# Performance work log

Measured on AMD Instinct MI355X. Metric: run time of the kernel, lower is better.

Reference implementation:

```python
import jax, jax.numpy as jnp
import numpy as np


def trilinear_sample(x, pts):
    """F.grid_sample 3D, mode='bilinear' (trilinear), padding_mode='border', align_corners=True.
    x: [B,C,D,H,W]; pts: [B,P,3] normalized coords in (x,y,z)=(W,H,D) order. Returns [B,C,P]."""
    B, C, D, H, W = x.shape

    def unnorm(g, size):
        # align_corners=True mapping, border padding = clamp coordinate
        return jnp.clip((g + 1.0) * 0.5 * (size - 1), 0.0, size - 1.0)

    ix = unnorm(pts[..., 0], W)
    iy = unnorm(pts[..., 1], H)
    iz = unnorm(pts[..., 2], D)
    x0 = jnp.floor(ix); y0 = jnp.floor(iy); z0 = jnp.floor(iz)
    fx = (ix - x0)[:, None, :]; fy = (iy - y0)[:, None, :]; fz = (iz - z0)[:, None, :]
    x0i = x0.astype(jnp.int32); y0i = y0.astype(jnp.int32); z0i = z0.astype(jnp.int32)
    x1i = jnp.minimum(x0i + 1, W - 1)
    y1i = jnp.minimum(y0i + 1, H - 1)
    z1i = jnp.minimum(z0i + 1, D - 1)

    xf = x.reshape(B, C, D * H * W)

    def gather(zi, yi, xi):
        idx = (zi * H + yi) * W + xi  # [B,P]
        return jnp.take_along_axis(xf, idx[:, None, :], axis=2)  # [B,C,P]

    wx0 = 1.0 - fx; wx1 = fx
    wy0 = 1.0 - fy; wy1 = fy
    wz0 = 1.0 - fz; wz1 = fz
    out = (gather(z0i, y0i, x0i) * wz0 * wy0 * wx0
           + gather(z0i, y0i, x1i) * wz0 * wy0 * wx1
           + gather(z0i, y1i, x0i) * wz0 * wy1 * wx0
           + gather(z0i, y1i, x1i) * wz0 * wy1 * wx1
           + gather(z1i, y0i, x0i) * wz1 * wy0 * wx0
           + gather(z1i, y0i, x1i) * wz1 * wy0 * wx1
           + gather(z1i, y1i, x0i) * wz1 * wy1 * wx0
           + gather(z1i, y1i, x1i) * wz1 * wy1 * wx1)
    return out


def setup_inputs() -> dict:
    key = jax.random.key(0)
    ks = jax.random.split(key, 12)
    B, C, G, N, K = 2, 64, 64, 50000, 8
    Cin = C + 3          # point_head / neighbour_head input channels
    Cd = C + 3 + 4       # delta conv input channels (features + coords + shape)
    s = 0.05
    x = jax.random.normal(ks[0], (B, C, G, G, G), jnp.float32)
    vertices = jax.random.uniform(ks[1], (B, N, 3), jnp.float32, -1.0, 1.0)
    shape_w = jax.random.normal(ks[2], (4, 4), jnp.float32) * s
    shape_b = jax.random.normal(ks[3], (4,), jnp.float32) * s
    # original init fills delta weights with 0; use small random values for a non-degenerate test
    delta_w = jax.random.normal(ks[4], (K * 3, Cd), jnp.float32) * 0.01
    delta_b = jax.random.normal(ks[5], (K * 3,), jnp.float32) * 0.01
    ph_w = jax.random.normal(ks[6], (C, Cin), jnp.float32) * s
    ph_b = jax.random.normal(ks[7], (C,), jnp.float32) * s
    nh1_w = jax.random.normal(ks[8], (C, Cin), jnp.float32) * s
    nh1_b = jax.random.normal(ks[9], (C,), jnp.float32) * s
    nh2_w = jax.random.normal(ks[10], (C, C, K + 1), jnp.float32) * s  # Conv2d kernel (1, K+1), no bias
    return {"x": x, "vertices": vertices, "shape_w": shape_w, "shape_b": shape_b,
            "delta_w": delta_w, "delta_b": delta_b, "ph_w": ph_w, "ph_b": ph_b,
            "nh1_w": nh1_w, "nh1_b": nh1_b, "nh2_w": nh2_w}


def reference(x, vertices, shape_w, shape_b, delta_w, delta_b, ph_w, ph_b, nh1_w, nh1_b, nh2_w):
    B, C, D, H, W = x.shape
    N = vertices.shape[1]
    K = delta_w.shape[0] // 3

    # sample point features
    xp = trilinear_sample(x, vertices)                                   # [B,C,N]
    cpoints = jnp.concatenate([xp, vertices.transpose(0, 2, 1)], axis=1)  # [B,C+3,N]

    # point head: 1x1 conv == per-point linear
    pfeat = jnp.einsum('oc,bcn->bno', ph_w, cpoints) + ph_b               # [B,N,C]

    # shape conditioning
    shape_vec = jnp.array([C, D, H, W], jnp.float32) @ shape_w.T + shape_b  # [4]
    sfeat = jnp.broadcast_to(shape_vec[None, :, None], (B, 4, N))
    feats = jnp.concatenate([cpoints, sfeat], axis=1)                     # [B,C+7,N]

    # learned neighbour offsets
    delta = (jnp.einsum('oc,bcn->bno', delta_w, feats) + delta_b).reshape(B, N, K, 3)
    nbrs = vertices[:, :, None, :] + delta                                # [B,N,K,3]

    # sample neighbour features
    xn = trilinear_sample(x, nbrs.reshape(B, N * K, 3)).reshape(B, C, N, K)
    cnb = jnp.concatenate([xn, nbrs.transpose(0, 3, 1, 2)], axis=1)       # [B,C+3,N,K]
    nin = jnp.concatenate([cpoints[..., None], cnb], axis=-1)             # [B,C+3,N,K+1]

    # neighbour head: 1x1 conv -> GELU -> (1,K+1) conv (reduces the K+1 axis)
    h = jax.nn.gelu(jnp.einsum('oc,bcnk->bonk', nh1_w, nin)
                    + nh1_b[None, :, None, None], approximate=False)
    nfeat = jnp.einsum('ock,bcnk->bno', nh2_w, h)                         # [B,N,C]

    return pfeat + nfeat
```

## Files before the change

### kernel.cpp

```cpp
#include <hip/hip_runtime.h>
#include <math.h>

constexpr int Bc = 2, Cc = 64, Nc = 50000, Kc = 8;
constexpr int PT = 16;
constexpr int NBLK = (Bc * Nc) / PT;

constexpr int BIAS_PH = 16;
constexpr int BIAS_N1 = 272;
constexpr int BIAS_DL = 528;
constexpr int B_PH  = 1024;
constexpr int B_N1  = 13312;
constexpr int B_DH  = 25600;
constexpr int B_DLO = 31744;
constexpr int B_N2  = 37888;
constexpr size_t XT_BYTE = 262144;
constexpr size_t XT_USHORTS = (size_t)Bc * 64 * 64 * 64 * 64;

using bf16x8 = __attribute__((ext_vector_type(8))) short;
using f32x4  = __attribute__((ext_vector_type(4))) float;

__device__ __forceinline__ float gelu_exact(float v) {
    return 0.5f * v * (1.0f + erff(v * 0.70710678118654752f));
}
__device__ __forceinline__ float gelu_fast(float v) {
    float u = fmaf(0.044715f * v * v, v, v);
    float s = 1.0f / (1.0f + __expf(-1.5957691216057308f * u));
    return v * s;
}
__device__ __forceinline__ ushort f2bf(float f) {
    unsigned u = __float_as_uint(f);
    unsigned r = (u + 0x7FFFu + ((u >> 16) & 1u)) >> 16;
    return (ushort)r;
}
__device__ __forceinline__ float bf2f(ushort u) {
    return __uint_as_float(((unsigned)u) << 16);
}
__device__ __forceinline__ float tri8(float v000, float v001, float v010, float v011,
                                      float v100, float v101, float v110, float v111,
                                      float fx, float fy, float fz) {
    float c00 = fmaf(fx, v001 - v000, v000);
    float c01 = fmaf(fx, v011 - v010, v010);
    float c10 = fmaf(fx, v101 - v100, v100);
    float c11 = fmaf(fx, v101 - v100, v100);
    c11 = fmaf(fx, v111 - v110, v110);
    float c0  = fmaf(fy, c01 - c00, c00);
    float c1  = fmaf(fy, c11 - c10, c10);
    return fmaf(fz, c1 - c0, c0);
}

__device__ __forceinline__ void precompute_pt(int* __restrict__ smp, int p,
                                              float nx, float ny, float nz) {
    float ix = fminf(fmaxf((nx + 1.0f) * 31.5f, 0.0f), 63.0f);
    float iy = fminf(fmaxf((ny + 1.0f) * 31.5f, 0.0f), 63.0f);
    float iz = fminf(fmaxf((nz + 1.0f) * 31.5f, 0.0f), 63.0f);
    float fx0 = floorf(ix), fy0 = floorf(iy), fz0 = floorf(iz);
    int x0 = (int)fx0, y0 = (int)fy0, z0 = (int)fz0;
    smp[p*8+0] = ((z0 << 12) + (y0 << 6) + x0) << 5;
    smp[p*8+1] = (x0 < 63) ? 32 : 0;
    smp[p*8+2] = (y0 < 63) ? 2048 : 0;
    smp[p*8+3] = (z0 < 63) ? 131072 : 0;
    smp[p*8+4] = __float_as_int(ix - fx0);
    smp[p*8+5] = __float_as_int(iy - fy0);
    smp[p*8+6] = __float_as_int(iz - fz0);
}

__device__ __forceinline__ void sample_pair2(const unsigned* __restrict__ xtb32,
                                             ushort* __restrict__ stage,
                                             const int* __restrict__ smp,
                                             int cp, int p) {
    const int* s = smp + p * 8;
    int base = s[0], dx = s[1], dy = s[2], dz = s[3];
    float fx = __int_as_float(s[4]);
    float fy = __int_as_float(s[5]);
    float fz = __int_as_float(s[6]);
    const unsigned* r = xtb32 + base + cp;
    unsigned u000 = r[0],       u001 = r[dx];
    unsigned u010 = r[dy],      u011 = r[dy + dx];
    unsigned u100 = r[dz],      u101 = r[dz + dx];
    unsigned u110 = r[dz + dy], u111 = r[dz + dy + dx];
    float sa = tri8(bf2f((ushort)u000), bf2f((ushort)u001),
                    bf2f((ushort)u010), bf2f((ushort)u011),
                    bf2f((ushort)u100), bf2f((ushort)u101),
                    bf2f((ushort)u110), bf2f((ushort)u111), fx, fy, fz);
    float sb = tri8(bf2f((ushort)(u000 >> 16)), bf2f((ushort)(u001 >> 16)),
                    bf2f((ushort)(u010 >> 16)), bf2f((ushort)(u011 >> 16)),
                    bf2f((ushort)(u100 >> 16)), bf2f((ushort)(u101 >> 16)),
                    bf2f((ushort)(u110 >> 16)), bf2f((ushort)(u111 >> 16)), fx, fy, fz);
    *(unsigned*)(stage + p * 104 + 2 * cp) =
        (unsigned)f2bf(sa) | ((unsigned)f2bf(sb) << 16);
}

__device__ __forceinline__ float sample_cm(const float* __restrict__ xb,
                                           float gx, float gy, float gz) {
    float ix = fminf(fmaxf((gx + 1.0f) * 31.5f, 0.0f), 63.0f);
    float iy = fminf(fmaxf((gy + 1.0f) * 31.5f, 0.0f), 63.0f);
    float iz = fminf(fmaxf((gz + 1.0f) * 31.5f, 0.0f), 63.0f);
    float fx0 = floorf(ix), fy0 = floorf(iy), fz0 = floorf(iz);
    int x0 = (int)fx0, y0 = (int)fy0, z0 = (int)fz0;
    float fx = ix - fx0, fy = iy - fy0, fz = iz - fz0;
    int x1 = (x0 < 63) ? x0 + 1 : 63;
    int dy = (y0 < 63) ? 64 : 0;
    int dz = (z0 < 63) ? 4096 : 0;
    const float* r = xb + ((z0 << 12) + (y0 << 6));
    float v000 = r[x0],           v001 = r[x1];
    float v010 = r[x0 + dy],      v011 = r[x1 + dy];
    float v100 = r[x0 + dz],      v101 = r[x1 + dz];
    float v110 = r[x0 + dy + dz], v111 = r[x1 + dy + dz];
    float c00 = fmaf(fx, v001 - v000, v000);
    float c01 = fmaf(fx, v011 - v010, v010);
    float c10 = fmaf(fx, v101 - v100, v100);
    float c11 = fmaf(fx, v111 - v110, v110);
    float c0  = fmaf(fy, c01 - c00, c00);
    float c1  = fmaf(fy, c11 - c10, c10);
    return fmaf(fz, c1 - c0, c0);
}

__global__ void sb_pack(const float* __restrict__ shape_w, const float* __restrict__ shape_b,
                        const float* __restrict__ delta_w, const float* __restrict__ delta_b,
                        const float* __restrict__ ph_w, const float* __restrict__ ph_b,
                        const float* __restrict__ nh1_w, const float* __restrict__ nh1_b,
                        const float* __restrict__ nh2_w, char* __restrict__ wsb) {
    int tid = blockIdx.x * blockDim.x + threadIdx.x;
    int nt  = gridDim.x * blockDim.x;
    float*  bph = (float*)(wsb + BIAS_PH);
    float*  bn1 = (float*)(wsb + BIAS_N1);
    float*  bdl = (float*)(wsb + BIAS_DL);
    ushort* wph = (ushort*)(wsb + B_PH);
    ushort* wn1 = (ushort*)(wsb + B_N1);
    ushort* wdh = (ushort*)(wsb + B_DH);
    ushort* wdl = (ushort*)(wsb + B_DLO);
    ushort* wn2 = (ushort*)(wsb + B_N2);

    for (int e = tid; e < 64; e += nt) { bph[e] = ph_b[e]; bn1[e] = nh1_b[e]; }
    for (int e = tid; e < 32; e += nt) {
        float v = 0.0f;
        if (e < 24) {
            v = delta_b[e];
#pragma unroll
            for (int i = 0; i < 4; ++i) {
                float sv = 64.0f * (shape_w[i*4] + shape_w[i*4+1] + shape_w[i*4+2] + shape_w[i*4+3])
                         + shape_b[i];
                v += sv * delta_w[e * 71 + 67 + i];
            }
        }
        bdl[e] = v;
    }
    for (int e = tid; e < 6144; e += nt) {
        int frag = e >> 9, lane = (e >> 3) & 63, j = e & 7;
        int kt = frag >> 2, n = frag & 3;
        int k = kt * 32 + ((lane >> 4) << 3) + j;
        int col = n * 16 + (lane & 15);
        wph[e] = (k < 67) ? f2bf(ph_w[col * 67 + k])  : (ushort)0;
        wn1[e] = (k < 67) ? f2bf(nh1_w[col * 67 + k]) : (ushort)0;
    }
    for (int e = tid; e < 3072; e += nt) {
        int frag = e >> 9, lane = (e >> 3) & 63, j = e & 7;
        int kt = frag >> 1, n = frag & 1;
        int k = kt * 32 + ((lane >> 4) << 3) + j;
        int col = n * 16 + (lane & 15);
        float w = (col < 24 && k < 67) ? delta_w[col * 71 + k] : 0.0f;
        ushort hi = f2bf(w);
        wdh[e] = hi;
        wdl[e] = f2bf(w - bf2f(hi));
    }
    for (int e = tid; e < 36864; e += nt) {
        int frag = e >> 9, lane = (e >> 3) & 63, j = e & 7;
        int c9 = frag >> 3, kt = (frag >> 2) & 1, n = frag & 3;
        int k = kt * 32 + ((lane >> 4) << 3) + j;
        int c = n * 16 + (lane & 15);
        wn2[e] = f2bf(nh2_w[(c * 64 + k) * 9 + c9]);
    }
}

__global__ __launch_bounds__(256) void sb_transpose(const float* __restrict__ x,
                                                    ushort* __restrict__ xt) {
    __shared__ float tile[64][65];
    int blk = blockIdx.x;
    int b = blk >> 12, zy = blk & 4095;
    const float* __restrict__ src = x + ((size_t)b << 24) + zy * 64;
    unsigned* __restrict__ dst32 = (unsigned*)(xt + ((size_t)b << 24) + (size_t)zy * 4096);
    int t = threadIdx.x;
    int xx = t & 63, c0 = t >> 6;
#pragma unroll
    for (int i = 0; i < 16; ++i) {
        int c = i * 4 + c0;
        tile[c][xx] = src[((size_t)c << 18) + xx];
    }
    __syncthreads();
    int cp = t & 31, xs0 = t >> 5;
#pragma unroll
    for (int i = 0; i < 8; ++i) {
        int xs = i * 8 + xs0;
        unsigned lo = f2bf(tile[cp * 2][xs]);
        unsigned hi = f2bf(tile[cp * 2 + 1][xs]);
        dst32[xs * 32 + cp] = lo | (hi << 16);
    }
}

__global__ __launch_bounds__(64, 6) void sb_main_mfma(
        const ushort* __restrict__ xt, const float* __restrict__ verts,
        const char* __restrict__ wsb, float* __restrict__ out) {
    __shared__ __align__(16) ushort stage[PT * 104];
    __shared__ __align__(16) ushort hst[PT * 72];
    __shared__ float pfs[PT * 64];
    __shared__ float cst[PT * 4];
    __shared__ float dls[PT * 32];
    __shared__ __align__(16) int smp[PT * 8];

    const int lane = threadIdx.x;
    const int l15 = lane & 15, lg = lane >> 4;
    const int half8 = (lane >> 5) * 8;
    const int cp = lane & 31;
    const int g0 = blockIdx.x * PT;
    const int b  = g0 / Nc;
    const unsigned* __restrict__ xtb32 = (const unsigned*)(xt + ((size_t)b << 24));

    const float*  bph = (const float*)(wsb + BIAS_PH);
    const float*  bn1 = (const float*)(wsb + BIAS_N1);
    const float*  bdl = (const float*)(wsb + BIAS_DL);
    const ushort* Wph = (const ushort*)(wsb + B_PH);
    const ushort* Wn1 = (const ushort*)(wsb + B_N1);
    const ushort* Wdh = (const ushort*)(wsb + B_DH);
    const ushort* Wdl = (const ushort*)(wsb + B_DLO);
    const ushort* Wn2 = (const ushort*)(wsb + B_N2);

#pragma unroll
    for (int i = 0; i < (PT * 104) / 64; ++i) stage[i * 64 + lane] = 0;

    if (lane < PT) {
        const float* vp = verts + (size_t)(g0 + lane) * 3;
        float x = vp[0], y = vp[1], z = vp[2];
        cst[lane*4+0] = x; cst[lane*4+1] = y; cst[lane*4+2] = z;
        uint4 cw;
        cw.x = (unsigned)f2bf(x) | ((unsigned)f2bf(y) << 16);
        cw.y = (unsigned)f2bf(z);
        cw.z = 0u; cw.w = 0u;
        *(uint4*)(stage + lane * 104 + 64) = cw;
        precompute_pt(smp, lane, x, y, z);
    }
    __syncthreads();

#pragma unroll 4
    for (int pp = 0; pp < 8; ++pp)
        sample_pair2(xtb32, stage, smp, cp, half8 + pp);
    __syncthreads();

    {
        f32x4 pf[4], dd[2];
#pragma unroll
        for (int n = 0; n < 4; ++n) {
            float bp = bph[n*16 + l15];
            pf[n] = (f32x4){bp, bp, bp, bp};
        }
#pragma unroll
        for (int n = 0; n < 2; ++n) {
            float bd = bdl[n*16 + l15];
            dd[n] = (f32x4){bd, bd, bd, bd};
        }
        __builtin_amdgcn_s_setprio(1);
#pragma unroll
        for (int kt = 0; kt < 3; ++kt) {
            bf16x8 a = *(const bf16x8*)(stage + l15 * 104 + kt * 32 + lg * 8);
#pragma unroll
            for (int n = 0; n < 4; ++n) {
                bf16x8 bw = *(const bf16x8*)(Wph + ((kt*4 + n) << 9) + lane * 8);
                pf[n] = __builtin_amdgcn_mfma_f32_16x16x32_bf16(a, bw, pf[n], 0, 0, 0);
            }
#pragma unroll
            for (int n = 0; n < 2; ++n) {
                bf16x8 bh = *(const bf16x8*)(Wdh + ((kt*2 + n) << 9) + lane * 8);
                dd[n] = __builtin_amdgcn_mfma_f32_16x16x32_bf16(a, bh, dd[n], 0, 0, 0);
                bf16x8 bl = *(const bf16x8*)(Wdl + ((kt*2 + n) << 9) + lane * 8);
                dd[n] = __builtin_amdgcn_mfma_f32_16x16x32_bf16(a, bl, dd[n], 0, 0, 0);
            }
        }
        __builtin_amdgcn_s_setprio(0);
#pragma unroll
        for (int n = 0; n < 2; ++n)
#pragma unroll
            for (int r = 0; r < 4; ++r)
                dls[(lg*4 + r) * 32 + n*16 + l15] = dd[n][r];
#pragma unroll
        for (int n = 0; n < 4; ++n)
#pragma unroll
            for (int r = 0; r < 4; ++r)
                pfs[(lg*4 + r) * 64 + n*16 + l15] = pf[n][r];
    }

    {
        f32x4 hh[4];
#pragma unroll
        for (int n = 0; n < 4; ++n) {
            float bh = bn1[n*16 + l15];
            hh[n] = (f32x4){bh, bh, bh, bh};
        }
        __builtin_amdgcn_s_setprio(1);
#pragma unroll
        for (int kt = 0; kt < 3; ++kt) {
            bf16x8 a = *(const bf16x8*)(stage + l15 * 104 + kt * 32 + lg * 8);
#pragma unroll
            for (int n = 0; n < 4; ++n) {
                bf16x8 b1 = *(const bf16x8*)(Wn1 + ((kt*4 + n) << 9) + lane * 8);
                hh[n] = __builtin_amdgcn_mfma_f32_16x16x32_bf16(a, b1, hh[n], 0, 0, 0);
            }
        }
        __builtin_amdgcn_s_setprio(0);
#pragma unroll
        for (int n = 0; n < 4; ++n)
#pragma unroll
            for (int r = 0; r < 4; ++r)
                hst[(lg*4 + r) * 72 + n*16 + l15] = f2bf(gelu_fast(hh[n][r]));
    }
    __syncthreads();

    f32x4 nf[4];
#pragma unroll
    for (int n = 0; n < 4; ++n) nf[n] = (f32x4){0.f, 0.f, 0.f, 0.f};
    __builtin_amdgcn_s_setprio(1);
#pragma unroll
    for (int kt = 0; kt < 2; ++kt) {
        bf16x8 a = *(const bf16x8*)(hst + l15 * 72 + kt * 32 + lg * 8);
#pragma unroll
        for (int n = 0; n < 4; ++n) {
            bf16x8 bw = *(const bf16x8*)(Wn2 + ((kt*4 + n) << 9) + lane * 8);
            nf[n] = __builtin_amdgcn_mfma_f32_16x16x32_bf16(a, bw, nf[n], 0, 0, 0);
        }
    }
    __builtin_amdgcn_s_setprio(0);

    for (int k = 0; k < Kc; ++k) {
        if (lane < PT) {
            float x = cst[lane*4+0] + dls[lane*32 + 3*k + 0];
            float y = cst[lane*4+1] + dls[lane*32 + 3*k + 1];
            float z = cst[lane*4+2] + dls[lane*32 + 3*k + 2];
            uint4 cw;
            cw.x = (unsigned)f2bf(x) | ((unsigned)f2bf(y) << 16);
            cw.y = (unsigned)f2bf(z);
            cw.z = 0u; cw.w = 0u;
            *(uint4*)(stage + lane * 104 + 64) = cw;
            precompute_pt(smp, lane, x, y, z);
        }
#pragma unroll 4
        for (int pp = 0; pp < 8; ++pp)
            sample_pair2(xtb32, stage, smp, cp, half8 + pp);
        __syncthreads();

        f32x4 hk[4];
#pragma unroll
        for (int n = 0; n < 4; ++n) {
            float bh = bn1[n*16 + l15];
            hk[n] = (f32x4){bh, bh, bh, bh};
        }
        __builtin_amdgcn_s_setprio(1);
#pragma unroll
        for (int kt = 0; kt < 3; ++kt) {
            bf16x8 a = *(const bf16x8*)(stage + l15 * 104 + kt * 32 + lg * 8);
#pragma unroll
            for (int n = 0; n < 4; ++n) {
                bf16x8 b1 = *(const bf16x8*)(Wn1 + ((kt*4 + n) << 9) + lane * 8);
                hk[n] = __builtin_amdgcn_mfma_f32_16x16x32_bf16(a, b1, hk[n], 0, 0, 0);
            }
        }
        __builtin_amdgcn_s_setprio(0);
#pragma unroll
        for (int n = 0; n < 4; ++n)
#pragma unroll
            for (int r = 0; r < 4; ++r)
                hst[(lg*4 + r) * 72 + n*16 + l15] = f2bf(gelu_fast(hk[n][r]));
        __syncthreads();

        const ushort* Wk = Wn2 + ((size_t)(k + 1) << 12);
        __builtin_amdgcn_s_setprio(1);
#pragma unroll
        for (int kt = 0; kt < 2; ++kt) {
            bf16x8 a = *(const bf16x8*)(hst + l15 * 72 + kt * 32 + lg * 8);
#pragma unroll
            for (int n = 0; n < 4; ++n) {
                bf16x8 bw = *(const bf16x8*)(Wk + ((kt*4 + n) << 9) + lane * 8);
                nf[n] = __builtin_amdgcn_mfma_f32_16x16x32_bf16(a, bw, nf[n], 0, 0, 0);
            }
        }
        __builtin_amdgcn_s_setprio(0);
    }

#pragma unroll
    for (int n = 0; n < 4; ++n)
#pragma unroll
        for (int r = 0; r < 4; ++r)
            out[(size_t)(g0 + lg*4 + r) * 64 + n*16 + l15] =
                pfs[(lg*4 + r) * 64 + n*16 + l15] + nf[n][r];
}

__global__ __launch_bounds__(64) void sb_fallback(
        const float* __restrict__ x, const float* __restrict__ verts,
        const float* __restrict__ shape_w, const float* __restrict__ shape_b,
        const float* __restrict__ delta_w, const float* __restrict__ delta_b,
        const float* __restrict__ ph_w, const float* __restrict__ ph_b,
        const float* __restrict__ nh1_w, const float* __restrict__ nh1_b,
        const float* __restrict__ nh2_w, float* __restrict__ out) {
    __shared__ float cp[72];
    __shared__ float hcol[64];
    __shared__ float dl[24];
    int lane = threadIdx.x;
    int g = blockIdx.x;
    int b = g / Nc;
    const float* xb = x + ((size_t)(b * 64 + lane) << 18);
    float vx = verts[g*3], vy = verts[g*3+1], vz = verts[g*3+2];
    cp[lane] = sample_cm(xb, vx, vy, vz);
    if (lane < 8) {
        float v = 0.0f;
        if      (lane == 0) v = vx;
        else if (lane == 1) v = vy;
        else if (lane == 2) v = vz;
        else if (lane < 7) {
            int i = lane - 3;
            v = 64.0f*(shape_w[i*4]+shape_w[i*4+1]+shape_w[i*4+2]+shape_w[i*4+3]) + shape_b[i];
        }
        cp[64 + lane] = v;
    }
    __syncthreads();
    float pfv = ph_b[lane];
    for (int j = 0; j < 67; ++j) pfv += ph_w[lane*67 + j] * cp[j];
    if (lane < 24) {
        float s = delta_b[lane];
        for (int j = 0; j < 71; ++j) s += delta_w[lane*71 + j] * cp[j];
        dl[lane] = s;
    }
    float h = nh1_b[lane];
    for (int j = 0; j < 67; ++j) h += nh1_w[lane*67 + j] * cp[j];
    hcol[lane] = gelu_exact(h);
    __syncthreads();
    float nfv = 0.0f;
    for (int c2 = 0; c2 < 64; ++c2) nfv += nh2_w[(lane*64 + c2)*9] * hcol[c2];
    for (int k = 0; k < 8; ++k) {
        __syncthreads();
        float nx = vx + dl[3*k], ny = vy + dl[3*k+1], nz = vz + dl[3*k+2];
        cp[lane] = sample_cm(xb, nx, ny, nz);
        if (lane < 3) cp[64 + lane] = (lane == 0) ? nx : (lane == 1) ? ny : nz;
        __syncthreads();
        float hv = nh1_b[lane];
        for (int j = 0; j < 67; ++j) hv += nh1_w[lane*67 + j] * cp[j];
        hcol[lane] = gelu_exact(hv);
        __syncthreads();
        for (int c2 = 0; c2 < 64; ++c2) nfv += nh2_w[(lane*64 + c2)*9 + k + 1] * hcol[c2];
    }
    out[(size_t)g * 64 + lane] = pfv + nfv;
}

extern "C" void kernel_launch(void* const* d_in, const int* in_sizes, int n_in,
                              void* d_out, int out_size, void* d_ws, size_t ws_size,
                              hipStream_t stream) {
    const float* x       = (const float*)d_in[0];
    const float* verts   = (const float*)d_in[1];
    const float* shape_w = (const float*)d_in[2];
    const float* shape_b = (const float*)d_in[3];
    const float* delta_w = (const float*)d_in[4];
    const float* delta_b = (const float*)d_in[5];
    const float* ph_w    = (const float*)d_in[6];
    const float* ph_b    = (const float*)d_in[7];
    const float* nh1_w   = (const float*)d_in[8];
    const float* nh1_b   = (const float*)d_in[9];
    const float* nh2_w   = (const float*)d_in[10];
    float* out = (float*)d_out;
    char*  wsb = (char*)d_ws;

    const size_t need = XT_BYTE + XT_USHORTS * 2;
    if (ws_size >= need) {
        ushort* xt = (ushort*)(wsb + XT_BYTE);
        sb_pack<<<96, 256, 0, stream>>>(shape_w, shape_b, delta_w, delta_b,
                                        ph_w, ph_b, nh1_w, nh1_b, nh2_w, wsb);
        sb_transpose<<<Bc * 4096, 256, 0, stream>>>(x, xt);
        sb_main_mfma<<<NBLK, 64, 0, stream>>>(xt, verts, wsb, out);
    } else {
        sb_fallback<<<Bc * Nc, 64, 0, stream>>>(x, verts, shape_w, shape_b, delta_w, delta_b,
                                                ph_w, ph_b, nh1_w, nh1_b, nh2_w, out);
    }
}
```

Baseline: 215.9 us.

## Prefetch trilinear corner gathers into LDS asynchronously, overlapping with MFMA work

Replaces the per-neighbour synchronous gather-and-interpolate with global_load_lds async copies of the corner values into an LDS raw buffer. The next neighbour's gathers are issued before the current neighbour's MFMA layers run, and sampling metadata is double-buffered. The point-linear result now stays in registers instead of LDS. This adds an LDS buffer and more live registers, and the occupancy hint is lowered from 6 to 4 waves.

```diff
diff --git a/kernel.cpp b/kernel.cpp
--- a/kernel.cpp
+++ b/kernel.cpp
@@ -41,11 +41,16 @@
     float c00 = fmaf(fx, v001 - v000, v000);
     float c01 = fmaf(fx, v011 - v010, v010);
     float c10 = fmaf(fx, v101 - v100, v100);
-    float c11 = fmaf(fx, v101 - v100, v100);
-    c11 = fmaf(fx, v111 - v110, v110);
+    float c11 = fmaf(fx, v111 - v110, v110);
     float c0  = fmaf(fy, c01 - c00, c00);
     float c1  = fmaf(fy, c11 - c10, c10);
     return fmaf(fz, c1 - c0, c0);
+}
+
+__device__ __forceinline__ void gll_dword(const unsigned* g, ushort* l) {
+    __builtin_amdgcn_global_load_lds(
+        (const __attribute__((address_space(1))) unsigned*)(g),
+        (__attribute__((address_space(3))) unsigned*)(l), 4, 0, 0);
 }
 
 __device__ __forceinline__ void precompute_pt(int* __restrict__ smp, int p,
@@ -55,39 +60,73 @@
     float iz = fminf(fmaxf((nz + 1.0f) * 31.5f, 0.0f), 63.0f);
     float fx0 = floorf(ix), fy0 = floorf(iy), fz0 = floorf(iz);
     int x0 = (int)fx0, y0 = (int)fy0, z0 = (int)fz0;
-    smp[p*8+0] = ((z0 << 12) + (y0 << 6) + x0) << 5;
-    smp[p*8+1] = (x0 < 63) ? 32 : 0;
-    smp[p*8+2] = (y0 < 63) ? 2048 : 0;
-    smp[p*8+3] = (z0 < 63) ? 131072 : 0;
-    smp[p*8+4] = __float_as_int(ix - fx0);
-    smp[p*8+5] = __float_as_int(iy - fy0);
-    smp[p*8+6] = __float_as_int(iz - fz0);
-}
-
-__device__ __forceinline__ void sample_pair2(const unsigned* __restrict__ xtb32,
-                                             ushort* __restrict__ stage,
-                                             const int* __restrict__ smp,
-                                             int cp, int p) {
-    const int* s = smp + p * 8;
-    int base = s[0], dx = s[1], dy = s[2], dz = s[3];
-    float fx = __int_as_float(s[4]);
-    float fy = __int_as_float(s[5]);
-    float fz = __int_as_float(s[6]);
-    const unsigned* r = xtb32 + base + cp;
-    unsigned u000 = r[0],       u001 = r[dx];
-    unsigned u010 = r[dy],      u011 = r[dy + dx];
-    unsigned u100 = r[dz],      u101 = r[dz + dx];
-    unsigned u110 = r[dz + dy], u111 = r[dz + dy + dx];
-    float sa = tri8(bf2f((ushort)u000), bf2f((ushort)u001),
-                    bf2f((ushort)u010), bf2f((ushort)u011),
-                    bf2f((ushort)u100), bf2f((ushort)u101),
-                    bf2f((ushort)u110), bf2f((ushort)u111), fx, fy, fz);
-    float sb = tri8(bf2f((ushort)(u000 >> 16)), bf2f((ushort)(u001 >> 16)),
-                    bf2f((ushort)(u010 >> 16)), bf2f((ushort)(u011 >> 16)),
-                    bf2f((ushort)(u100 >> 16)), bf2f((ushort)(u101 >> 16)),
-                    bf2f((ushort)(u110 >> 16)), bf2f((ushort)(u111 >> 16)), fx, fy, fz);
-    *(unsigned*)(stage + p * 104 + 2 * cp) =
-        (unsigned)f2bf(sa) | ((unsigned)f2bf(sb) << 16);
+    int* s = smp + p * 12;
+    s[0] = ((z0 << 12) + (y0 << 6) + x0) << 5;
+    s[1] = (x0 < 63) ? 32 : 0;
+    s[2] = (y0 < 63) ? 2048 : 0;
+    s[3] = (z0 < 63) ? 131072 : 0;
+    s[4] = __float_as_int(ix - fx0);
+    s[5] = __float_as_int(iy - fy0);
+    s[6] = __float_as_int(iz - fz0);
+    s[7] = __float_as_int(nx);
+    s[8] = __float_as_int(ny);
+    s[9] = __float_as_int(nz);
+}
+
+__device__ __forceinline__ void issue_all(const unsigned* __restrict__ xtb32,
+                                          ushort* __restrict__ raw,
+                                          const int* __restrict__ smp, int lane) {
+    int xs = (lane >= 32);
+    int chp = lane & 31;
+#pragma unroll 4
+    for (int p = 0; p < PT; ++p) {
+        const int* s = smp + p * 12;
+        int base = s[0], dxo = s[1], dyo = s[2], dzo = s[3];
+        const unsigned* g = xtb32 + base + (xs ? dxo : 0) + chp;
+        ushort* rp = raw + p * 512;
+        gll_dword(g,             rp);
+        gll_dword(g + dyo,       rp + 128);
+        gll_dword(g + dzo,       rp + 256);
+        gll_dword(g + dzo + dyo, rp + 384);
+    }
+}
+
+__device__ __forceinline__ void combine_col(const ushort* __restrict__ raw,
+                                            ushort* __restrict__ stage,
+                                            const int* __restrict__ smp,
+                                            int cp, int half8, int lane) {
+#pragma unroll 4
+    for (int pp = 0; pp < 8; ++pp) {
+        int p = half8 + pp;
+        const unsigned* D = (const unsigned*)(raw + p * 512);
+        const int* s = smp + p * 12;
+        float fx = __int_as_float(s[4]);
+        float fy = __int_as_float(s[5]);
+        float fz = __int_as_float(s[6]);
+        unsigned u000 = D[cp],        u001 = D[32 + cp];
+        unsigned u010 = D[64 + cp],   u011 = D[96 + cp];
+        unsigned u100 = D[128 + cp],  u101 = D[160 + cp];
+        unsigned u110 = D[192 + cp],  u111 = D[224 + cp];
+        float sa = tri8(bf2f((ushort)u000), bf2f((ushort)u001),
+                        bf2f((ushort)u010), bf2f((ushort)u011),
+                        bf2f((ushort)u100), bf2f((ushort)u101),
+                        bf2f((ushort)u110), bf2f((ushort)u111), fx, fy, fz);
+        float sb = tri8(bf2f((ushort)(u000 >> 16)), bf2f((ushort)(u001 >> 16)),
+                        bf2f((ushort)(u010 >> 16)), bf2f((ushort)(u011 >> 16)),
+                        bf2f((ushort)(u100 >> 16)), bf2f((ushort)(u101 >> 16)),
+                        bf2f((ushort)(u110 >> 16)), bf2f((ushort)(u111 >> 16)), fx, fy, fz);
+        *(unsigned*)(stage + p * 104 + 2 * cp) =
+            (unsigned)f2bf(sa) | ((unsigned)f2bf(sb) << 16);
+    }
+    if (lane < PT) {
+        const int* s = smp + lane * 12;
+        uint4 cw;
+        cw.x = (unsigned)f2bf(__int_as_float(s[7])) |
+               ((unsigned)f2bf(__int_as_float(s[8])) << 16);
+        cw.y = (unsigned)f2bf(__int_as_float(s[9]));
+        cw.z = 0u; cw.w = 0u;
+        *(uint4*)(stage + lane * 104 + 64) = cw;
+    }
 }
 
 __device__ __forceinline__ float sample_cm(const float* __restrict__ xb,
@@ -102,17 +141,8 @@
     int dy = (y0 < 63) ? 64 : 0;
     int dz = (z0 < 63) ? 4096 : 0;
     const float* r = xb + ((z0 << 12) + (y0 << 6));
-    float v000 = r[x0],           v001 = r[x1];
-    float v010 = r[x0 + dy],      v011 = r[x1 + dy];
-    float v100 = r[x0 + dz],      v101 = r[x1 + dz];
-    float v110 = r[x0 + dy + dz], v111 = r[x1 + dy + dz];
-    float c00 = fmaf(fx, v001 - v000, v000);
-    float c01 = fmaf(fx, v011 - v010, v010);
-    float c10 = fmaf(fx, v101 - v100, v100);
-    float c11 = fmaf(fx, v111 - v110, v110);
-    float c0  = fmaf(fy, c01 - c00, c00);
-    float c1  = fmaf(fy, c11 - c10, c10);
-    return fmaf(fz, c1 - c0, c0);
+    return tri8(r[x0], r[x1], r[x0+dy], r[x1+dy],
+                r[x0+dz], r[x1+dz], r[x0+dy+dz], r[x1+dy+dz], fx, fy, fz);
 }
 
 __global__ void sb_pack(const float* __restrict__ shape_w, const float* __restrict__ shape_b,
@@ -197,15 +227,15 @@
     }
 }
 
-__global__ __launch_bounds__(64, 6) void sb_main_mfma(
+__global__ __launch_bounds__(64, 4) void sb_main_mfma(
         const ushort* __restrict__ xt, const float* __restrict__ verts,
         const char* __restrict__ wsb, float* __restrict__ out) {
     __shared__ __align__(16) ushort stage[PT * 104];
     __shared__ __align__(16) ushort hst[PT * 72];
-    __shared__ float pfs[PT * 64];
+    __shared__ __align__(16) ushort raw[PT * 512];
     __shared__ float cst[PT * 4];
     __shared__ float dls[PT * 32];
-    __shared__ __align__(16) int smp[PT * 8];
+    __shared__ __align__(16) int smp[2][PT * 12];
 
     const int lane = threadIdx.x;
     const int l15 = lane & 15, lg = lane >> 4;
@@ -231,22 +261,18 @@
         const float* vp = verts + (size_t)(g0 + lane) * 3;
         float x = vp[0], y = vp[1], z = vp[2];
         cst[lane*4+0] = x; cst[lane*4+1] = y; cst[lane*4+2] = z;
-        uint4 cw;
-        cw.x = (unsigned)f2bf(x) | ((unsigned)f2bf(y) << 16);
-        cw.y = (unsigned)f2bf(z);
-        cw.z = 0u; cw.w = 0u;
-        *(uint4*)(stage + lane * 104 + 64) = cw;
-        precompute_pt(smp, lane, x, y, z);
-    }
-    __syncthreads();
-
-#pragma unroll 4
-    for (int pp = 0; pp < 8; ++pp)
-        sample_pair2(xtb32, stage, smp, cp, half8 + pp);
-    __syncthreads();
-
+        precompute_pt(smp[0], lane, x, y, z);
+    }
+    __syncthreads();
+    issue_all(xtb32, raw, smp[0], lane);
+    __syncthreads();
+
+    combine_col(raw, stage, smp[0], cp, half8, lane);
+    __syncthreads();
+
+    f32x4 pf[4];
     {
-        f32x4 pf[4], dd[2];
+        f32x4 dd[2];
 #pragma unroll
         for (int n = 0; n < 4; ++n) {
             float bp = bph[n*16 + l15];
@@ -280,12 +306,17 @@
 #pragma unroll
             for (int r = 0; r < 4; ++r)
                 dls[(lg*4 + r) * 32 + n*16 + l15] = dd[n][r];
-#pragma unroll
-        for (int n = 0; n < 4; ++n)
-#pragma unroll
-            for (int r = 0; r < 4; ++r)
-                pfs[(lg*4 + r) * 64 + n*16 + l15] = pf[n][r];
-    }
+    }
+    __syncthreads();
+
+    if (lane < PT) {
+        precompute_pt(smp[1], lane,
+                      cst[lane*4+0] + dls[lane*32 + 0],
+                      cst[lane*4+1] + dls[lane*32 + 1],
+                      cst[lane*4+2] + dls[lane*32 + 2]);
+    }
+    __syncthreads();
+    issue_all(xtb32, raw, smp[1], lane);
 
     {
         f32x4 hh[4];
@@ -328,22 +359,19 @@
     }
     __builtin_amdgcn_s_setprio(0);
 
-    for (int k = 0; k < Kc; ++k) {
-        if (lane < PT) {
-            float x = cst[lane*4+0] + dls[lane*32 + 3*k + 0];
-            float y = cst[lane*4+1] + dls[lane*32 + 3*k + 1];
-            float z = cst[lane*4+2] + dls[lane*32 + 3*k + 2];
-            uint4 cw;
-            cw.x = (unsigned)f2bf(x) | ((unsigned)f2bf(y) << 16);
-            cw.y = (unsigned)f2bf(z);
-            cw.z = 0u; cw.w = 0u;
-            *(uint4*)(stage + lane * 104 + 64) = cw;
-            precompute_pt(smp, lane, x, y, z);
-        }
-#pragma unroll 4
-        for (int pp = 0; pp < 8; ++pp)
-            sample_pair2(xtb32, stage, smp, cp, half8 + pp);
+    for (int k = 1; k <= Kc; ++k) {
+        const int* sc = smp[k & 1];
         __syncthreads();
+
+        combine_col(raw, stage, sc, cp, half8, lane);
+        if (k < Kc && lane < PT) {
+            precompute_pt(smp[(k + 1) & 1], lane,
+                          cst[lane*4+0] + dls[lane*32 + 3*k + 0],
+                          cst[lane*4+1] + dls[lane*32 + 3*k + 1],
+                          cst[lane*4+2] + dls[lane*32 + 3*k + 2]);
+        }
+        __syncthreads();
+        if (k < Kc) issue_all(xtb32, raw, smp[(k + 1) & 1], lane);
 
         f32x4 hk[4];
 #pragma unroll
@@ -369,7 +397,7 @@
                 hst[(lg*4 + r) * 72 + n*16 + l15] = f2bf(gelu_fast(hk[n][r]));
         __syncthreads();
 
-        const ushort* Wk = Wn2 + ((size_t)(k + 1) << 12);
+        const ushort* Wk = Wn2 + ((size_t)k << 12);
         __builtin_amdgcn_s_setprio(1);
 #pragma unroll
         for (int kt = 0; kt < 2; ++kt) {
@@ -387,8 +415,7 @@
     for (int n = 0; n < 4; ++n)
 #pragma unroll
         for (int r = 0; r < 4; ++r)
-            out[(size_t)(g0 + lg*4 + r) * 64 + n*16 + l15] =
-                pfs[(lg*4 + r) * 64 + n*16 + l15] + nf[n][r];
+            out[(size_t)(g0 + lg*4 + r) * 64 + n*16 + l15] = pf[n][r] + nf[n][r];
 }
 
 __global__ __launch_bounds__(64) void sb_fallback(
```

New measurement: 266.0 us. 1.23x slower.
